# Optimization experiments

Hardware: AMD Instinct MI355X
Metric: run time of the kernel (lower is better)

Reference implementation:

```python
import jax, jax.numpy as jnp
import numpy as np

D_MODEL = 1024
MEM_HEADS = 4
MEM_KNN = 32
KEY_DIM = 288
VALUE_DIM = 512
Q_RANK = 512
MEM_N_KEYS = 512
TOTAL_KEYS = MEM_N_KEYS * MEM_N_KEYS        # 262144
NUM_BUCKETS = int(np.log2(TOTAL_KEYS))      # 18
BUCKET_DIM = KEY_DIM // NUM_BUCKETS         # 16
BATCH, SEQ = 4, 512


def setup_inputs() -> dict:
    key = jax.random.key(0)
    ks = jax.random.split(key, 7)
    bound = 1.0 / np.sqrt(BUCKET_DIM)
    return {
        "x": jax.random.normal(ks[0], (BATCH, SEQ, D_MODEL), dtype=jnp.float32),
        "keys": jax.random.uniform(ks[1], (MEM_HEADS, NUM_BUCKETS, 2, BUCKET_DIM),
                                   minval=-bound, maxval=bound, dtype=jnp.float32),
        "qd_w": jax.random.normal(ks[2], (Q_RANK, D_MODEL), dtype=jnp.float32) * (1.0 / np.sqrt(D_MODEL)),
        "qd_b": jnp.zeros((Q_RANK,), dtype=jnp.float32),
        "qu_w": jax.random.normal(ks[3], (MEM_HEADS * KEY_DIM, Q_RANK), dtype=jnp.float32) * (1.0 / np.sqrt(Q_RANK)),
        "values": jax.random.normal(ks[4], (TOTAL_KEYS, VALUE_DIM), dtype=jnp.float32) * (VALUE_DIM ** -0.5),
        "vp_w": jax.random.normal(ks[5], (D_MODEL, VALUE_DIM), dtype=jnp.float32) * (1.0 / np.sqrt(VALUE_DIM)),
    }


def _get_indices(query, keys, knn):
    # query: [rows_tok, H, key_dim] flattened per head below. Here query comes
    # in as [N*H, key_dim] reshaped to [N, H, M, bucket_dim].
    N = query.shape[0]
    q = query.reshape(N, MEM_HEADS, NUM_BUCKETS, BUCKET_DIM)
    local = jnp.einsum("nhmd,hmcd->nhmc", q, keys)          # [N,H,M,2]
    s0, s1 = local[..., 0], local[..., 1]
    best_bits = s1 > s0                                      # [N,H,M]
    best_scores = jnp.maximum(s0, s1).sum(-1)                # [N,H]
    deltas = jnp.abs(s0 - s1)                                # [N,H,M]
    bit_weights = (1 << jnp.arange(NUM_BUCKETS, dtype=jnp.int32))
    best_codes = (best_bits.astype(jnp.int32) * bit_weights).sum(-1)  # [N,H]

    rows = N * MEM_HEADS
    deltas = deltas.reshape(rows, NUM_BUCKETS)
    best_scores = best_scores.reshape(rows, 1)
    best_codes = best_codes.reshape(rows, 1)
    knn_eff = min(knn, 1 << NUM_BUCKETS)

    penalties = jnp.zeros((rows, 1), dtype=jnp.float32)
    masks = jnp.zeros((rows, 1), dtype=jnp.int32)
    # Trellis search: unrolled Python loop over a small fixed bucket count (18);
    # candidate width grows 2,4,... then saturates at 2*knn -> static shapes.
    for t in range(NUM_BUCKETS):
        cand_pen = jnp.concatenate([penalties, penalties + deltas[:, t:t + 1]], axis=1)
        cand_msk = jnp.concatenate([masks, masks ^ bit_weights[t]], axis=1)
        step_k = min(knn_eff, cand_pen.shape[1])
        neg_pen, keep = jax.lax.top_k(-cand_pen, step_k)     # smallest penalties, sorted asc
        penalties = -neg_pen
        masks = jnp.take_along_axis(cand_msk, keep, axis=1)
    return best_scores - penalties, best_codes ^ masks        # [rows,knn], [rows,knn]


def reference(x, keys, qd_w, qd_b, qu_w, values, vp_w):
    B, S, D = x.shape
    N = B * S
    x_flat = x.reshape(N, D)
    q = (x_flat @ qd_w.T + qd_b) @ qu_w.T                    # [N, H*key_dim]
    scores, indices = _get_indices(q.reshape(N, MEM_HEADS, KEY_DIM), keys, MEM_KNN)
    scores = jax.nn.softmax(scores, axis=-1)                 # [N*H, knn]
    indices = indices.reshape(N, MEM_HEADS * MEM_KNN)
    scores = scores.reshape(N, MEM_HEADS * MEM_KNN)
    gathered = values[indices]                               # [N, H*knn, value_dim]
    y = jnp.einsum("nk,nkd->nd", scores, gathered)           # embedding_bag mode='sum'
    y = y @ vp_w.T                                           # value_proj (value_dim != d_model)
    return y.reshape(B, S, D_MODEL)
```

## Files before the change

kernel.cpp:

```cpp
#include <hip/hip_runtime.h>
#include <math.h>

#define D_MODEL 1024
#define MEM_HEADS 4
#define KNN 32
#define KEY_DIM 288
#define VALUE_DIM 512
#define Q_RANK 512
#define NUM_BUCKETS 18
#define BUCKET_DIM 16
#define NTOK 2048
#define ROWS (NTOK * MEM_HEADS)
#define QDIM (MEM_HEADS * KEY_DIM)

typedef __attribute__((ext_vector_type(8))) short bfrag;
typedef __attribute__((ext_vector_type(4))) float f32x4;

__device__ __forceinline__ unsigned short f2bf(float x) {
    unsigned int u = __builtin_bit_cast(unsigned int, x);
    u += 0x7FFFu + ((u >> 16) & 1u);
    return (unsigned short)(u >> 16);
}
__device__ __forceinline__ float bf2f(unsigned short h) {
    unsigned int u = ((unsigned int)h) << 16;
    return __builtin_bit_cast(float, u);
}

#define LSTR 40
template<int MODE>
__global__ __launch_bounds__(256) void gemm_nt_split(
    const float* __restrict__ A, const float* __restrict__ B,
    const float* __restrict__ bias, float* __restrict__ C,
    int M, int N, int K)
{
    __shared__ __align__(16) unsigned short As[MODE][64][LSTR];
    __shared__ __align__(16) unsigned short Bs[MODE][64][LSTR];

    const int tid  = threadIdx.x;
    const int bm   = blockIdx.y * 64;
    const int bn   = blockIdx.x * 64;
    const int wave = tid >> 6;
    const int lane = tid & 63;
    const int wr   = wave & 1;
    const int wc   = wave >> 1;
    const int l15  = lane & 15;
    const int quad = lane >> 4;

    const int sr = tid >> 2;
    const int sg = tid & 3;

    f32x4 acc[2][2];
#pragma unroll
    for (int i = 0; i < 2; ++i)
#pragma unroll
        for (int j = 0; j < 2; ++j) acc[i][j] = (f32x4){0.f, 0.f, 0.f, 0.f};

    const float* Ap = A + (size_t)(bm + sr) * K + sg * 8;
    const float* Bp = B + (size_t)(bn + sr) * K + sg * 8;

    for (int k0 = 0; k0 < K; k0 += 32) {
        const float4 a0 = *(const float4*)(Ap + k0);
        const float4 a1 = *(const float4*)(Ap + k0 + 4);
        const float4 b0 = *(const float4*)(Bp + k0);
        const float4 b1 = *(const float4*)(Bp + k0 + 4);

        __syncthreads();
        {
            const float va[8] = {a0.x,a0.y,a0.z,a0.w, a1.x,a1.y,a1.z,a1.w};
            const float vb[8] = {b0.x,b0.y,b0.z,b0.w, b1.x,b1.y,b1.z,b1.w};
            bfrag ha[MODE], hb[MODE];
#pragma unroll
            for (int i = 0; i < 8; ++i) {
                float xa = va[i], xb = vb[i];
#pragma unroll
                for (int s = 0; s < MODE; ++s) {
                    const unsigned short sa = f2bf(xa), sb = f2bf(xb);
                    ha[s][i] = (short)sa; hb[s][i] = (short)sb;
                    xa -= bf2f(sa);       xb -= bf2f(sb);
                }
            }
#pragma unroll
            for (int s = 0; s < MODE; ++s) {
                *(bfrag*)&As[s][sr][sg * 8] = ha[s];
                *(bfrag*)&Bs[s][sr][sg * 8] = hb[s];
            }
        }
        __syncthreads();

        bfrag af[MODE][2], bf[MODE][2];
#pragma unroll
        for (int t = 0; t < 2; ++t) {
            const int mr = wr * 32 + t * 16 + l15;
            const int nr = wc * 32 + t * 16 + l15;
#pragma unroll
            for (int s = 0; s < MODE; ++s) {
                af[s][t] = *(const bfrag*)&As[s][mr][quad * 8];
                bf[s][t] = *(const bfrag*)&Bs[s][nr][quad * 8];
            }
        }
#pragma unroll
        for (int mt = 0; mt < 2; ++mt)
#pragma unroll
            for (int nt = 0; nt < 2; ++nt) {
                f32x4 c = acc[mt][nt];
                c = __builtin_amdgcn_mfma_f32_16x16x32_bf16(af[0][mt], bf[0][nt], c, 0, 0, 0);
                c = __builtin_amdgcn_mfma_f32_16x16x32_bf16(af[0][mt], bf[1][nt], c, 0, 0, 0);
                c = __builtin_amdgcn_mfma_f32_16x16x32_bf16(af[1][mt], bf[0][nt], c, 0, 0, 0);
                if (MODE == 3) {
                    c = __builtin_amdgcn_mfma_f32_16x16x32_bf16(af[1][mt], bf[1][nt], c, 0, 0, 0);
                    c = __builtin_amdgcn_mfma_f32_16x16x32_bf16(af[0][mt], bf[2][nt], c, 0, 0, 0);
                    c = __builtin_amdgcn_mfma_f32_16x16x32_bf16(af[2][mt], bf[0][nt], c, 0, 0, 0);
                }
                acc[mt][nt] = c;
            }
    }

#pragma unroll
    for (int nt = 0; nt < 2; ++nt) {
        const int col = bn + wc * 32 + nt * 16 + l15;
        const float bv = bias ? bias[col] : 0.f;
#pragma unroll
        for (int mt = 0; mt < 2; ++mt) {
            const int rowb = bm + wr * 32 + mt * 16 + quad * 4;
#pragma unroll
            for (int g = 0; g < 4; ++g)
                C[(size_t)(rowb + g) * N + col] = acc[mt][nt][g] + bv;
        }
    }
}

__global__ __launch_bounds__(64) void trellis_kernel(
    const float* __restrict__ q, const float* __restrict__ keys,
    float* __restrict__ sc_out, int* __restrict__ idx_out)
{
    __shared__ float s_keys[MEM_HEADS * NUM_BUCKETS * 2 * BUCKET_DIM];
    __shared__ float penB[2][KNN][64];
    __shared__ int   mskB[2][KNN][64];

    const int tid = threadIdx.x;
    for (int i = tid; i < MEM_HEADS * NUM_BUCKETS * 2 * BUCKET_DIM; i += 64)
        s_keys[i] = keys[i];
    __syncthreads();

    const int r = blockIdx.x * 64 + tid;
    const int h = r & 3;
    const float* qr = q + (size_t)r * KEY_DIM;

    float dlt[NUM_BUCKETS];
    int code = 0;
#pragma unroll
    for (int m = 0; m < NUM_BUCKETS; ++m) {
        const float* km = s_keys + h * (NUM_BUCKETS * 32) + m * 32;
        const float4 q0 = *(const float4*)(qr + m * BUCKET_DIM);
        const float4 q1 = *(const float4*)(qr + m * BUCKET_DIM + 4);
        const float4 q2 = *(const float4*)(qr + m * BUCKET_DIM + 8);
        const float4 q3 = *(const float4*)(qr + m * BUCKET_DIM + 12);
        const float qv[16] = {q0.x,q0.y,q0.z,q0.w, q1.x,q1.y,q1.z,q1.w,
                              q2.x,q2.y,q2.z,q2.w, q3.x,q3.y,q3.z,q3.w};
        float s0 = 0.f, s1 = 0.f;
#pragma unroll
        for (int d = 0; d < BUCKET_DIM; ++d) {
            s0 += qv[d] * km[d];
            s1 += qv[d] * km[16 + d];
        }
        dlt[m] = fabsf(s0 - s1);
        if (s1 > s0) code |= (1 << m);
    }

    penB[0][0][tid] = 0.f;
    mskB[0][0][tid] = 0;
    int nb = 1, cur = 0;
#pragma unroll
    for (int t = 0; t < NUM_BUCKETS; ++t) {
        const float d = dlt[t];
        const int nk = min(KNN, nb * 2);
        const int nxt = cur ^ 1;
        int i = 0, j = 0;
        for (int o = 0; o < nk; ++o) {
            const float pa = (i < nb) ? penB[cur][i][tid] : 3.4e38f;
            const float pb = (j < nb) ? (penB[cur][j][tid] + d) : 3.4e38f;
            if (pa <= pb) {
                penB[nxt][o][tid] = pa;
                mskB[nxt][o][tid] = mskB[cur][i][tid];
                ++i;
            } else {
                penB[nxt][o][tid] = pb;
                mskB[nxt][o][tid] = mskB[cur][j][tid] ^ (1 << t);
                ++j;
            }
        }
        nb = nk;
        cur = nxt;
    }

    float e[KNN];
    float Z = 0.f;
#pragma unroll
    for (int i = 0; i < KNN; ++i) {
        e[i] = expf(-penB[cur][i][tid]);
        Z += e[i];
    }
    const float inv = 1.0f / Z;
#pragma unroll
    for (int i = 0; i < KNN; ++i) {
        sc_out[(size_t)r * KNN + i]  = e[i] * inv;
        idx_out[(size_t)r * KNN + i] = code ^ mskB[cur][i][tid];
    }
}

__global__ __launch_bounds__(128) void gather_kernel(
    const float* __restrict__ sc, const int* __restrict__ idx,
    const float* __restrict__ values, float* __restrict__ y)
{
    __shared__ float s_s[MEM_HEADS * KNN];
    __shared__ int   s_i[MEM_HEADS * KNN];
    const int n = blockIdx.x;
    const int t = threadIdx.x;
    s_s[t] = sc[(size_t)n * 128 + t];
    s_i[t] = idx[(size_t)n * 128 + t];
    __syncthreads();

    float4 acc = {0.f, 0.f, 0.f, 0.f};
#pragma unroll 8
    for (int k = 0; k < 128; ++k) {
        const float4 v = *(const float4*)(values + (size_t)s_i[k] * VALUE_DIM + t * 4);
        const float w = s_s[k];
        acc.x += w * v.x; acc.y += w * v.y;
        acc.z += w * v.z; acc.w += w * v.w;
    }
    *(float4*)(y + (size_t)n * VALUE_DIM + t * 4) = acc;
}

extern "C" void kernel_launch(void* const* d_in, const int* in_sizes, int n_in,
                              void* d_out, int out_size, void* d_ws, size_t ws_size,
                              hipStream_t stream)
{
    (void)in_sizes; (void)n_in; (void)out_size; (void)ws_size;
    const float* x      = (const float*)d_in[0];
    const float* keys   = (const float*)d_in[1];
    const float* qd_w   = (const float*)d_in[2];
    const float* qd_b   = (const float*)d_in[3];
    const float* qu_w   = (const float*)d_in[4];
    const float* values = (const float*)d_in[5];
    const float* vp_w   = (const float*)d_in[6];
    float* out = (float*)d_out;

    float* q_mid = (float*)d_ws;
    float* q     = q_mid + (size_t)NTOK * Q_RANK;
    float* sc    = q + (size_t)NTOK * QDIM;
    int*   idx   = (int*)(sc + (size_t)ROWS * KNN);
    float* y     = (float*)(idx + (size_t)ROWS * KNN);

    gemm_nt_split<3><<<dim3(Q_RANK / 64, NTOK / 64), 256, 0, stream>>>(
        x, qd_w, qd_b, q_mid, NTOK, Q_RANK, D_MODEL);
    gemm_nt_split<3><<<dim3(QDIM / 64, NTOK / 64), 256, 0, stream>>>(
        q_mid, qu_w, nullptr, q, NTOK, QDIM, Q_RANK);
    trellis_kernel<<<ROWS / 64, 64, 0, stream>>>(q, keys, sc, idx);
    gather_kernel<<<NTOK, 128, 0, stream>>>(sc, idx, values, y);
    gemm_nt_split<2><<<dim3(D_MODEL / 64, NTOK / 64), 256, 0, stream>>>(
        y, vp_w, nullptr, out, NTOK, D_MODEL, VALUE_DIM);
}
```

Before: 868.7 us.

## Presplit GEMM operands into bf16 planes once instead of per tile

Adds a prep kernel that splits x and all weight matrices into 2-3 bf16 planes up front. Producer kernels (first GEMM epilogue and gather) now emit split bf16 planes directly, so the GEMM inner loop only loads and stores the planes into shared memory. This removes redundant f32-to-bf16 split arithmetic that each tile block repeated for every shared operand. In exchange it adds an extra launch and extra memory traffic for writing and rereading the planes.

```diff
diff --git a/kernel.cpp b/kernel.cpp
--- a/kernel.cpp
+++ b/kernel.cpp
@@ -13,28 +13,56 @@
 #define ROWS (NTOK * MEM_HEADS)
 #define QDIM (MEM_HEADS * KEY_DIM)
 
+typedef unsigned short u16;
 typedef __attribute__((ext_vector_type(8))) short bfrag;
 typedef __attribute__((ext_vector_type(4))) float f32x4;
-
-__device__ __forceinline__ unsigned short f2bf(float x) {
+typedef __attribute__((ext_vector_type(4))) unsigned short u16x4;
+
+__device__ __forceinline__ u16 f2bf(float x) {
     unsigned int u = __builtin_bit_cast(unsigned int, x);
     u += 0x7FFFu + ((u >> 16) & 1u);
-    return (unsigned short)(u >> 16);
-}
-__device__ __forceinline__ float bf2f(unsigned short h) {
+    return (u16)(u >> 16);
+}
+__device__ __forceinline__ float bf2f(u16 h) {
     unsigned int u = ((unsigned int)h) << 16;
     return __builtin_bit_cast(float, u);
 }
 
+__global__ __launch_bounds__(256) void split_prep(
+    const float* __restrict__ x, const float* __restrict__ qdw,
+    const float* __restrict__ quw, const float* __restrict__ vpw,
+    u16* __restrict__ xs, u16* __restrict__ qds,
+    u16* __restrict__ qus, u16* __restrict__ vps)
+{
+    const float* src; u16* dst; int n; int ns;
+    switch (blockIdx.y) {
+        case 0:  src = x;   dst = xs;  n = NTOK * D_MODEL;     ns = 3; break;
+        case 1:  src = qdw; dst = qds; n = Q_RANK * D_MODEL;   ns = 3; break;
+        case 2:  src = quw; dst = qus; n = QDIM * Q_RANK;      ns = 3; break;
+        default: src = vpw; dst = vps; n = D_MODEL * VALUE_DIM; ns = 2; break;
+    }
+    const int n4 = n >> 2;
+    for (int i = blockIdx.x * 256 + threadIdx.x; i < n4; i += gridDim.x * 256) {
+        const float4 v = ((const float4*)src)[i];
+        float c0 = v.x, c1 = v.y, c2 = v.z, c3 = v.w;
+        for (int s = 0; s < ns; ++s) {
+            const u16 h0 = f2bf(c0), h1 = f2bf(c1), h2 = f2bf(c2), h3 = f2bf(c3);
+            const u16x4 h = {h0, h1, h2, h3};
+            *(u16x4*)(dst + (size_t)s * n + (size_t)i * 4) = h;
+            c0 -= bf2f(h0); c1 -= bf2f(h1); c2 -= bf2f(h2); c3 -= bf2f(h3);
+        }
+    }
+}
+
 #define LSTR 40
-template<int MODE>
-__global__ __launch_bounds__(256) void gemm_nt_split(
-    const float* __restrict__ A, const float* __restrict__ B,
-    const float* __restrict__ bias, float* __restrict__ C,
-    int M, int N, int K)
-{
-    __shared__ __align__(16) unsigned short As[MODE][64][LSTR];
-    __shared__ __align__(16) unsigned short Bs[MODE][64][LSTR];
+template<int MODE, int OUTS>
+__global__ __launch_bounds__(256) void gemm_nt_pre(
+    const u16* __restrict__ A, const u16* __restrict__ B,
+    const float* __restrict__ bias, float* __restrict__ Cf,
+    u16* __restrict__ Cs, int M, int N, int K)
+{
+    __shared__ __align__(16) u16 As[MODE][64][LSTR];
+    __shared__ __align__(16) u16 Bs[MODE][64][LSTR];
 
     const int tid  = threadIdx.x;
     const int bm   = blockIdx.y * 64;
@@ -55,35 +83,24 @@
 #pragma unroll
         for (int j = 0; j < 2; ++j) acc[i][j] = (f32x4){0.f, 0.f, 0.f, 0.f};
 
-    const float* Ap = A + (size_t)(bm + sr) * K + sg * 8;
-    const float* Bp = B + (size_t)(bn + sr) * K + sg * 8;
+    const size_t pA = (size_t)M * K;
+    const size_t pB = (size_t)N * K;
+    const u16* Ap = A + (size_t)(bm + sr) * K + sg * 8;
+    const u16* Bp = B + (size_t)(bn + sr) * K + sg * 8;
 
     for (int k0 = 0; k0 < K; k0 += 32) {
-        const float4 a0 = *(const float4*)(Ap + k0);
-        const float4 a1 = *(const float4*)(Ap + k0 + 4);
-        const float4 b0 = *(const float4*)(Bp + k0);
-        const float4 b1 = *(const float4*)(Bp + k0 + 4);
+        bfrag la[MODE], lb[MODE];
+#pragma unroll
+        for (int s = 0; s < MODE; ++s) {
+            la[s] = *(const bfrag*)(Ap + s * pA + k0);
+            lb[s] = *(const bfrag*)(Bp + s * pB + k0);
+        }
 
         __syncthreads();
-        {
-            const float va[8] = {a0.x,a0.y,a0.z,a0.w, a1.x,a1.y,a1.z,a1.w};
-            const float vb[8] = {b0.x,b0.y,b0.z,b0.w, b1.x,b1.y,b1.z,b1.w};
-            bfrag ha[MODE], hb[MODE];
-#pragma unroll
-            for (int i = 0; i < 8; ++i) {
-                float xa = va[i], xb = vb[i];
-#pragma unroll
-                for (int s = 0; s < MODE; ++s) {
-                    const unsigned short sa = f2bf(xa), sb = f2bf(xb);
-                    ha[s][i] = (short)sa; hb[s][i] = (short)sb;
-                    xa -= bf2f(sa);       xb -= bf2f(sb);
-                }
-            }
-#pragma unroll
-            for (int s = 0; s < MODE; ++s) {
-                *(bfrag*)&As[s][sr][sg * 8] = ha[s];
-                *(bfrag*)&Bs[s][sr][sg * 8] = hb[s];
-            }
+#pragma unroll
+        for (int s = 0; s < MODE; ++s) {
+            *(bfrag*)&As[s][sr][sg * 8] = la[s];
+            *(bfrag*)&Bs[s][sr][sg * 8] = lb[s];
         }
         __syncthreads();
 
@@ -123,8 +140,20 @@
         for (int mt = 0; mt < 2; ++mt) {
             const int rowb = bm + wr * 32 + mt * 16 + quad * 4;
 #pragma unroll
-            for (int g = 0; g < 4; ++g)
-                C[(size_t)(rowb + g) * N + col] = acc[mt][nt][g] + bv;
+            for (int g = 0; g < 4; ++g) {
+                float c = acc[mt][nt][g] + bv;
+                const size_t off = (size_t)(rowb + g) * N + col;
+                if (OUTS == 0) {
+                    Cf[off] = c;
+                } else {
+#pragma unroll
+                    for (int s = 0; s < OUTS; ++s) {
+                        const u16 h = f2bf(c);
+                        Cs[(size_t)s * ((size_t)M * N) + off] = h;
+                        c -= bf2f(h);
+                    }
+                }
+            }
         }
     }
 }
@@ -210,7 +239,7 @@
 
 __global__ __launch_bounds__(128) void gather_kernel(
     const float* __restrict__ sc, const int* __restrict__ idx,
-    const float* __restrict__ values, float* __restrict__ y)
+    const float* __restrict__ values, u16* __restrict__ ys)
 {
     __shared__ float s_s[MEM_HEADS * KNN];
     __shared__ int   s_i[MEM_HEADS * KNN];
@@ -228,7 +257,19 @@
         acc.x += w * v.x; acc.y += w * v.y;
         acc.z += w * v.z; acc.w += w * v.w;
     }
-    *(float4*)(y + (size_t)n * VALUE_DIM + t * 4) = acc;
+
+    float c[4] = {acc.x, acc.y, acc.z, acc.w};
+    u16x4 h0, h1;
+#pragma unroll
+    for (int cc = 0; cc < 4; ++cc) {
+        const u16 a = f2bf(c[cc]);
+        h0[cc] = a;
+        const float rres = c[cc] - bf2f(a);
+        h1[cc] = f2bf(rres);
+    }
+    const size_t off = (size_t)n * VALUE_DIM + t * 4;
+    *(u16x4*)(ys + off) = h0;
+    *(u16x4*)(ys + (size_t)NTOK * VALUE_DIM + off) = h1;
 }
 
 extern "C" void kernel_launch(void* const* d_in, const int* in_sizes, int n_in,
@@ -245,18 +286,25 @@
     const float* vp_w   = (const float*)d_in[6];
     float* out = (float*)d_out;
 
-    float* q_mid = (float*)d_ws;
-    float* q     = q_mid + (size_t)NTOK * Q_RANK;
-    float* sc    = q + (size_t)NTOK * QDIM;
-    int*   idx   = (int*)(sc + (size_t)ROWS * KNN);
-    float* y     = (float*)(idx + (size_t)ROWS * KNN);
-
-    gemm_nt_split<3><<<dim3(Q_RANK / 64, NTOK / 64), 256, 0, stream>>>(
-        x, qd_w, qd_b, q_mid, NTOK, Q_RANK, D_MODEL);
-    gemm_nt_split<3><<<dim3(QDIM / 64, NTOK / 64), 256, 0, stream>>>(
-        q_mid, qu_w, nullptr, q, NTOK, QDIM, Q_RANK);
+    char* w = (char*)d_ws;
+    u16* xs  = (u16*)w;  w += (size_t)NTOK * D_MODEL * 2 * 3;
+    u16* qds = (u16*)w;  w += (size_t)Q_RANK * D_MODEL * 2 * 3;
+    u16* qus = (u16*)w;  w += (size_t)QDIM * Q_RANK * 2 * 3;
+    u16* vps = (u16*)w;  w += (size_t)D_MODEL * VALUE_DIM * 2 * 2;
+    u16* qms = (u16*)w;  w += (size_t)NTOK * Q_RANK * 2 * 3;
+    u16* ys  = (u16*)w;  w += (size_t)NTOK * VALUE_DIM * 2 * 2;
+    float* q   = (float*)w; w += (size_t)NTOK * QDIM * 4;
+    float* sc  = (float*)w; w += (size_t)ROWS * KNN * 4;
+    int*   idx = (int*)w;
+
+    split_prep<<<dim3(256, 4), 256, 0, stream>>>(
+        x, qd_w, qu_w, vp_w, xs, qds, qus, vps);
+    gemm_nt_pre<3, 3><<<dim3(Q_RANK / 64, NTOK / 64), 256, 0, stream>>>(
+        xs, qds, qd_b, nullptr, qms, NTOK, Q_RANK, D_MODEL);
+    gemm_nt_pre<3, 0><<<dim3(QDIM / 64, NTOK / 64), 256, 0, stream>>>(
+        qms, qus, nullptr, q, nullptr, NTOK, QDIM, Q_RANK);
     trellis_kernel<<<ROWS / 64, 64, 0, stream>>>(q, keys, sc, idx);
-    gather_kernel<<<NTOK, 128, 0, stream>>>(sc, idx, values, y);
-    gemm_nt_split<2><<<dim3(D_MODEL / 64, NTOK / 64), 256, 0, stream>>>(
-        y, vp_w, nullptr, out, NTOK, D_MODEL, VALUE_DIM);
-}
+    gather_kernel<<<NTOK, 128, 0, stream>>>(sc, idx, values, ys);
+    gemm_nt_pre<2, 0><<<dim3(D_MODEL / 64, NTOK / 64), 256, 0, stream>>>(
+        ys, vps, nullptr, out, nullptr, NTOK, D_MODEL, VALUE_DIM);
+}
```

Measured after the change: 1.011 ms. 1.16x slower.

## Replace LDS merge loop in trellis search with register bitonic merge

Applied to the files above, without the earlier changes.

The per-row top-k trellis step was a data-dependent sequential merge of two sorted lists stored in shared memory. It becomes a fixed, branch-free bitonic merge held entirely in registers: the reversed shifted list is combined elementwise with the original, then sorted by a 5-stage compare-exchange network. This removes LDS traffic and divergent control flow, at the cost of more compare/select instructions and much higher register pressure (pen/msk plus np/nm arrays of 32 each).

```diff
diff --git a/kernel.cpp b/kernel.cpp
--- a/kernel.cpp
+++ b/kernel.cpp
@@ -134,8 +134,6 @@
     float* __restrict__ sc_out, int* __restrict__ idx_out)
 {
     __shared__ float s_keys[MEM_HEADS * NUM_BUCKETS * 2 * BUCKET_DIM];
-    __shared__ float penB[2][KNN][64];
-    __shared__ int   mskB[2][KNN][64];
 
     const int tid = threadIdx.x;
     for (int i = tid; i < MEM_HEADS * NUM_BUCKETS * 2 * BUCKET_DIM; i += 64)
@@ -167,44 +165,58 @@
         if (s1 > s0) code |= (1 << m);
     }
 
-    penB[0][0][tid] = 0.f;
-    mskB[0][0][tid] = 0;
-    int nb = 1, cur = 0;
+    float pen[KNN];
+    int   msk[KNN];
+    pen[0] = 0.f; msk[0] = 0;
+#pragma unroll
+    for (int i = 1; i < KNN; ++i) { pen[i] = 3.0e38f; msk[i] = 0; }
+
 #pragma unroll
     for (int t = 0; t < NUM_BUCKETS; ++t) {
-        const float d = dlt[t];
-        const int nk = min(KNN, nb * 2);
-        const int nxt = cur ^ 1;
-        int i = 0, j = 0;
-        for (int o = 0; o < nk; ++o) {
-            const float pa = (i < nb) ? penB[cur][i][tid] : 3.4e38f;
-            const float pb = (j < nb) ? (penB[cur][j][tid] + d) : 3.4e38f;
-            if (pa <= pb) {
-                penB[nxt][o][tid] = pa;
-                mskB[nxt][o][tid] = mskB[cur][i][tid];
-                ++i;
-            } else {
-                penB[nxt][o][tid] = pb;
-                mskB[nxt][o][tid] = mskB[cur][j][tid] ^ (1 << t);
-                ++j;
-            }
-        }
-        nb = nk;
-        cur = nxt;
+        const float d   = dlt[t];
+        const int   bit = 1 << t;
+        float np[KNN]; int nm[KNN];
+#pragma unroll
+        for (int i = 0; i < KNN; ++i) {
+            const float pb = pen[KNN - 1 - i] + d;
+            const int   mb = msk[KNN - 1 - i] ^ bit;
+            const bool  ta = pen[i] <= pb;
+            np[i] = ta ? pen[i] : pb;
+            nm[i] = ta ? msk[i] : mb;
+        }
+#pragma unroll
+        for (int k = 16; k >= 1; k >>= 1) {
+#pragma unroll
+            for (int i = 0; i < KNN; ++i) {
+                if ((i & k) == 0) {
+                    const int jj = i | k;
+                    const float a = np[i], b = np[jj];
+                    const bool  ta = a <= b;
+                    const float lo = ta ? a : b;
+                    const float hi = ta ? b : a;
+                    const int   ml = ta ? nm[i] : nm[jj];
+                    const int   mh = ta ? nm[jj] : nm[i];
+                    np[i] = lo; np[jj] = hi;
+                    nm[i] = ml; nm[jj] = mh;
+                }
+            }
+        }
+#pragma unroll
+        for (int i = 0; i < KNN; ++i) { pen[i] = np[i]; msk[i] = nm[i]; }
     }
 
     float e[KNN];
     float Z = 0.f;
 #pragma unroll
     for (int i = 0; i < KNN; ++i) {
-        e[i] = expf(-penB[cur][i][tid]);
+        e[i] = expf(-pen[i]);
         Z += e[i];
     }
     const float inv = 1.0f / Z;
 #pragma unroll
     for (int i = 0; i < KNN; ++i) {
         sc_out[(size_t)r * KNN + i]  = e[i] * inv;
-        idx_out[(size_t)r * KNN + i] = code ^ mskB[cur][i][tid];
+        idx_out[(size_t)r * KNN + i] = code ^ msk[i];
     }
 }
 
```

New measurement: 1.414 ms. +62.8%, slower.

## Parallelize trellis top-k search across wave lanes with bitonic shuffle merge

Applied to the files above, without the earlier changes.

The trellis kernel previously ran one thread per query row, doing a serial 32-element merge in shared memory for each of 18 buckets, which left the GPU mostly idle with only 128 small blocks. Each row is now handled by 32 lanes. Bucket scores are computed one bucket per lane, and every step uses a min against the reversed shifted list followed by a shuffle-based bitonic merge, so no shared-memory scratch is needed. The grid grows to 1024 blocks of 256 threads and the keys get a padded shared-memory layout. Tie ordering between equal penalties may differ from the serial merge.

```diff
diff --git a/kernel.cpp b/kernel.cpp
--- a/kernel.cpp
+++ b/kernel.cpp
@@ -129,32 +129,36 @@
     }
 }
 
-__global__ __launch_bounds__(64) void trellis_kernel(
+#define KPAD 34
+__global__ __launch_bounds__(256) void trellis_kernel(
     const float* __restrict__ q, const float* __restrict__ keys,
     float* __restrict__ sc_out, int* __restrict__ idx_out)
 {
-    __shared__ float s_keys[MEM_HEADS * NUM_BUCKETS * 2 * BUCKET_DIM];
-    __shared__ float penB[2][KNN][64];
-    __shared__ int   mskB[2][KNN][64];
+    __shared__ float s_keys[MEM_HEADS * NUM_BUCKETS * KPAD];
 
     const int tid = threadIdx.x;
-    for (int i = tid; i < MEM_HEADS * NUM_BUCKETS * 2 * BUCKET_DIM; i += 64)
-        s_keys[i] = keys[i];
+    for (int i = tid; i < MEM_HEADS * NUM_BUCKETS * 32; i += 256) {
+        const int row = i >> 5, d = i & 31;
+        s_keys[row * KPAD + d] = keys[i];
+    }
     __syncthreads();
 
-    const int r = blockIdx.x * 64 + tid;
-    const int h = r & 3;
-    const float* qr = q + (size_t)r * KEY_DIM;
-
-    float dlt[NUM_BUCKETS];
-    int code = 0;
-#pragma unroll
-    for (int m = 0; m < NUM_BUCKETS; ++m) {
-        const float* km = s_keys + h * (NUM_BUCKETS * 32) + m * 32;
-        const float4 q0 = *(const float4*)(qr + m * BUCKET_DIM);
-        const float4 q1 = *(const float4*)(qr + m * BUCKET_DIM + 4);
-        const float4 q2 = *(const float4*)(qr + m * BUCKET_DIM + 8);
-        const float4 q3 = *(const float4*)(qr + m * BUCKET_DIM + 12);
+    const int wave = tid >> 6;
+    const int lane = tid & 63;
+    const int sub  = lane >> 5;
+    const int l    = lane & 31;
+    const int r    = blockIdx.x * 8 + wave * 2 + sub;
+    const int h    = r & 3;
+
+    float dlt = 0.f;
+    int bit_l = 0;
+    if (l < NUM_BUCKETS) {
+        const float* km = s_keys + (h * NUM_BUCKETS + l) * KPAD;
+        const float* qr = q + (size_t)r * KEY_DIM + l * BUCKET_DIM;
+        const float4 q0 = *(const float4*)(qr);
+        const float4 q1 = *(const float4*)(qr + 4);
+        const float4 q2 = *(const float4*)(qr + 8);
+        const float4 q3 = *(const float4*)(qr + 12);
         const float qv[16] = {q0.x,q0.y,q0.z,q0.w, q1.x,q1.y,q1.z,q1.w,
                               q2.x,q2.y,q2.z,q2.w, q3.x,q3.y,q3.z,q3.w};
         float s0 = 0.f, s1 = 0.f;
@@ -163,49 +167,44 @@
             s0 += qv[d] * km[d];
             s1 += qv[d] * km[16 + d];
         }
-        dlt[m] = fabsf(s0 - s1);
-        if (s1 > s0) code |= (1 << m);
-    }
-
-    penB[0][0][tid] = 0.f;
-    mskB[0][0][tid] = 0;
-    int nb = 1, cur = 0;
+        dlt = fabsf(s0 - s1);
+        if (s1 > s0) bit_l = 1 << l;
+    }
+    int code = bit_l;
+#pragma unroll
+    for (int k = 16; k >= 1; k >>= 1) code |= __shfl_xor(code, k);
+
+    float pen = (l == 0) ? 0.f : 3.0e38f;
+    int   msk = 0;
 #pragma unroll
     for (int t = 0; t < NUM_BUCKETS; ++t) {
-        const float d = dlt[t];
-        const int nk = min(KNN, nb * 2);
-        const int nxt = cur ^ 1;
-        int i = 0, j = 0;
-        for (int o = 0; o < nk; ++o) {
-            const float pa = (i < nb) ? penB[cur][i][tid] : 3.4e38f;
-            const float pb = (j < nb) ? (penB[cur][j][tid] + d) : 3.4e38f;
-            if (pa <= pb) {
-                penB[nxt][o][tid] = pa;
-                mskB[nxt][o][tid] = mskB[cur][i][tid];
-                ++i;
-            } else {
-                penB[nxt][o][tid] = pb;
-                mskB[nxt][o][tid] = mskB[cur][j][tid] ^ (1 << t);
-                ++j;
-            }
-        }
-        nb = nk;
-        cur = nxt;
-    }
-
-    float e[KNN];
-    float Z = 0.f;
-#pragma unroll
-    for (int i = 0; i < KNN; ++i) {
-        e[i] = expf(-penB[cur][i][tid]);
-        Z += e[i];
-    }
+        const float d   = __shfl(dlt, t, 32);
+        const int   bit = 1 << t;
+        const float pr = __shfl_xor(pen, 31);
+        const int   mr = __shfl_xor(msk, 31);
+        const float pb = pr + d;
+        const bool  ta = (pen <= pb);
+        float p = ta ? pen : pb;
+        int   m = ta ? msk : (mr ^ bit);
+#pragma unroll
+        for (int k = 16; k >= 1; k >>= 1) {
+            const float op = __shfl_xor(p, k);
+            const int   om = __shfl_xor(m, k);
+            const bool  lower = ((l & k) == 0);
+            const bool  take  = lower ? (op < p) : (op > p);
+            p = take ? op : p;
+            m = take ? om : m;
+        }
+        pen = p; msk = m;
+    }
+
+    const float e = expf(-pen);
+    float Z = e;
+#pragma unroll
+    for (int k = 16; k >= 1; k >>= 1) Z += __shfl_xor(Z, k);
     const float inv = 1.0f / Z;
-#pragma unroll
-    for (int i = 0; i < KNN; ++i) {
-        sc_out[(size_t)r * KNN + i]  = e[i] * inv;
-        idx_out[(size_t)r * KNN + i] = code ^ mskB[cur][i][tid];
-    }
+    sc_out[(size_t)r * KNN + l]  = e * inv;
+    idx_out[(size_t)r * KNN + l] = code ^ msk;
 }
 
 __global__ __launch_bounds__(128) void gather_kernel(
@@ -255,7 +254,7 @@
         x, qd_w, qd_b, q_mid, NTOK, Q_RANK, D_MODEL);
     gemm_nt_split<3><<<dim3(QDIM / 64, NTOK / 64), 256, 0, stream>>>(
         q_mid, qu_w, nullptr, q, NTOK, QDIM, Q_RANK);
-    trellis_kernel<<<ROWS / 64, 64, 0, stream>>>(q, keys, sc, idx);
+    trellis_kernel<<<ROWS / 8, 256, 0, stream>>>(q, keys, sc, idx);
     gather_kernel<<<NTOK, 128, 0, stream>>>(sc, idx, values, y);
     gemm_nt_split<2><<<dim3(D_MODEL / 64, NTOK / 64), 256, 0, stream>>>(
         y, vp_w, nullptr, out, NTOK, D_MODEL, VALUE_DIM);
```

Measured after the change: 784.9 us. 1.11x faster.
